# Kernel tuning notes

Measured on AMD Instinct MI355X. Metric: run time of the kernel, lower is better.

## Reference

```python
import jax, jax.numpy as jnp
import numpy as np

N_NODES = 40000
N_EDGES = 640000
D_FEAT = 128


def setup_inputs() -> dict:
    key = jax.random.key(0)
    k1, k2, k3, k4, k5 = jax.random.split(key, 5)
    x = jax.random.normal(k1, (N_NODES, D_FEAT), dtype=jnp.float32)
    edge_rows = jax.random.randint(k2, (N_EDGES,), 0, N_NODES, dtype=jnp.int32)
    edge_cols = jax.random.randint(k3, (N_EDGES,), 0, N_NODES, dtype=jnp.int32)
    adj_vals = jax.random.uniform(k4, (N_EDGES,), dtype=jnp.float32)
    bias = jax.random.normal(k5, (D_FEAT,), dtype=jnp.float32)
    return {"x": x, "edge_rows": edge_rows, "edge_cols": edge_cols,
            "adj_vals": adj_vals, "bias": bias}


def reference(x, edge_rows, edge_cols, adj_vals, bias):
    # SpMM: out[r] = sum_e adj_vals[e] * x[edge_cols[e]] for edges with row r
    msgs = adj_vals[:, None] * x[edge_cols]                    # [E, D]
    agg = jax.ops.segment_sum(msgs, edge_rows, num_segments=N_NODES)  # [E,D]->[N,D]
    # degree = sparse row-sum of adj values
    deg = jax.ops.segment_sum(adj_vals, edge_rows, num_segments=N_NODES)  # [N]
    deg = deg[:, None]
    # mean aggregation; rows with zero degree give NaN in torch, masked to 0
    out = jnp.where(deg == 0, 0.0, agg / jnp.where(deg == 0, 1.0, deg))
    return out + bias
```

## Files before the change

### kernel.cpp

```cpp
#include <hip/hip_runtime.h>

#define N_NODES 40000
#define N_EDGES 640000
#define D_FEAT  128
#define CAP     32
#define OCAP    8192
#define NSLICE  8
#define SLICE_NODES 5000
#define NSUB    16
#define NBIN    (NSLICE * NSUB)
#define BIN2    28
#define STAGE_BLOCKS 625
#define HEAVY_BLOCKS NBIN
#define RANGE_MAX 313
#define CONV_BLOCKS_1K 1250
#define SCAN_BLOCK 256
#define N_SCAN_BLOCKS ((N_NODES + SCAN_BLOCK - 1) / SCAN_BLOCK)

typedef float    f32x4 __attribute__((ext_vector_type(4)));

__device__ __forceinline__ unsigned bf16r(float f) {
    unsigned u = __float_as_uint(f);
    return (u + 0x7FFFu + ((u >> 16) & 1u)) >> 16;
}


__global__ __launch_bounds__(256) void stage_kernel(
    const int*   __restrict__ rows,
    const int*   __restrict__ cols,
    const float* __restrict__ vals,
    int*          __restrict__ ocount,
    int2*         __restrict__ overflow,
    uint2*        __restrict__ queue)
{
    __shared__ int   cnt[NBIN];
    __shared__ uint2 bin[NBIN][BIN2];

    for (int i = threadIdx.x; i < NBIN; i += 256) cnt[i] = 0;
    __syncthreads();

    int vidx = blockIdx.x * 256 + threadIdx.x;
    int4   r4 = ((const int4*)  rows)[vidx];
    int4   c4 = ((const int4*)  cols)[vidx];
    float4 v4 = ((const float4*)vals)[vidx];
    int    rr[4] = { r4.x, r4.y, r4.z, r4.w };
    int    cc[4] = { c4.x, c4.y, c4.z, c4.w };
    float  vv[4] = { v4.x, v4.y, v4.z, v4.w };

    #pragma unroll
    for (int j = 0; j < 4; ++j) {
        int r = rr[j];
        unsigned p = ((unsigned)cc[j] << 16) | bf16r(vv[j]);
        int sl  = r / SLICE_NODES;
        int lr  = r - sl * SLICE_NODES;
        int sub = (lr * NSUB) / SLICE_NODES;
        int bi  = sl * NSUB + sub;
        int idx = atomicAdd(&cnt[bi], 1);
        if (idx < BIN2) {
            bin[bi][idx] = make_uint2(p, (unsigned)r);
        } else {
            int o = atomicAdd(ocount, 1);
            if (o < OCAP) overflow[o] = make_int2(r, (int)p);
        }
    }
    __syncthreads();

    int b = blockIdx.x;
    for (int idx = threadIdx.x; idx < NBIN * BIN2; idx += 256) {
        unsigned bi   = (unsigned)idx / BIN2;
        unsigned slot = (unsigned)idx - bi * BIN2;
        int c = min(cnt[bi], BIN2);
        uint2 rec = (slot < (unsigned)c) ? bin[bi][slot]
                                         : make_uint2(0u, 0xFFFFFFFFu);
        queue[((size_t)bi * STAGE_BLOCKS + b) * BIN2 + slot] = rec;
    }
}

__global__ __launch_bounds__(1024) void consume_kernel(
    const float* __restrict__ x,
    const uint2* __restrict__ queue,
    int*          __restrict__ cursors,
    unsigned*     __restrict__ bucket,
    int*          __restrict__ ocount,
    int2*         __restrict__ overflow,
    uint2*        __restrict__ xbf)
{
    int b = blockIdx.x;
    if (b < HEAVY_BLOCKS) {
        int s = b & 7;
        int j = b >> 3;
        int loc0  = (j * SLICE_NODES + NSUB - 1) / NSUB;
        int loc1  = ((j + 1) * SLICE_NODES + NSUB - 1) / NSUB;
        int range = loc1 - loc0;
        int node0 = s * SLICE_NODES + loc0;

        __shared__ int      lcnt[RANGE_MAX];
        __shared__ unsigned lbuck[RANGE_MAX][CAP];

        for (int i = threadIdx.x; i < range; i += 1024) lcnt[i] = 0;
        __syncthreads();

        const uint2* q = queue + (size_t)(s * NSUB + j) * STAGE_BLOCKS * BIN2;
        const int n = STAGE_BLOCKS * BIN2;
        for (int i = threadIdx.x; i < n; i += 1024) {
            uint2 rec = q[i];
            unsigned ln = rec.y - (unsigned)node0;
            if (ln < (unsigned)range) {
                int idx = atomicAdd(&lcnt[ln], 1);
                if (idx < CAP) lbuck[ln][idx] = rec.x;
                else { int o = atomicAdd(ocount, 1);
                       if (o < OCAP) overflow[o] = make_int2((int)rec.y, (int)rec.x); }
            }
        }
        __syncthreads();

        for (int i = threadIdx.x; i < range; i += 1024)
            cursors[node0 + i] = lcnt[i];
        const unsigned* lb = &lbuck[0][0];
        unsigned* gb = bucket + (size_t)node0 * CAP;
        for (int w = threadIdx.x; w < range * CAP; w += 1024)
            gb[w] = lb[w];
        return;
    }
    int idx = (b - HEAVY_BLOCKS) * 1024 + threadIdx.x;
    float4 f = ((const float4*)x)[idx];
    uint2 o;
    o.x = bf16r(f.x) | (bf16r(f.y) << 16);
    o.y = bf16r(f.z) | (bf16r(f.w) << 16);
    xbf[idx] = o;
}

__global__ __launch_bounds__(256, 8) void gather_bf_kernel(
    const uint2*    __restrict__ xbf,
    const int*      __restrict__ cursors,
    const unsigned* __restrict__ bucket,
    const int2*     __restrict__ overflow,
    const float*    __restrict__ bias,
    float*          __restrict__ out)
{
    int b    = blockIdx.x;
    int hw   = threadIdx.x >> 5;
    int lane = threadIdx.x & 31;
    int node = (b & 7) * SLICE_NODES + (b >> 3) * 8 + hw;

    int k = min(cursors[node], CAP);
    const unsigned* base = bucket + (unsigned)node * CAP;

    unsigned ent = (lane < k) ? base[lane] : 0xFFFFFFFFu;

    #pragma unroll
    for (int kk = 2; kk <= 32; kk <<= 1) {
        #pragma unroll
        for (int j = kk >> 1; j > 0; j >>= 1) {
            unsigned other = __shfl_xor(ent, j, 64);
            bool up      = ((lane & kk) == 0);
            bool lower   = ((lane & j) == 0);
            unsigned mn  = min(ent, other), mx = max(ent, other);
            ent = (up == lower) ? mn : mx;
        }
    }

    int wb = threadIdx.x & 32;

    float4 acc0 = make_float4(0.f, 0.f, 0.f, 0.f);
    float4 acc1 = make_float4(0.f, 0.f, 0.f, 0.f);
    float  deg  = 0.f;

    #define ACC(P_, W_, A_)  {                                             \
        float _v = __uint_as_float((P_) << 16);                            \
        float _f0 = __uint_as_float((W_).x << 16);                         \
        float _f1 = __uint_as_float((W_).x & 0xFFFF0000u);                 \
        float _f2 = __uint_as_float((W_).y << 16);                         \
        float _f3 = __uint_as_float((W_).y & 0xFFFF0000u);                 \
        deg += _v;                                                         \
        A_.x += _v * _f0; A_.y += _v * _f1;                                \
        A_.z += _v * _f2; A_.w += _v * _f3; }

    #define PROC(E_, A_)  {                                                \
        unsigned _en = (E_);                                               \
        uint2 _wv = xbf[(_en >> 16) * 32u + (unsigned)lane];               \
        ACC(_en, _wv, A_); }

    int e = 0;
    for (; e + 8 <= k; e += 8) {
        unsigned p0 = __shfl(ent, wb + e,     64);
        unsigned p1 = __shfl(ent, wb + e + 1, 64);
        unsigned p2 = __shfl(ent, wb + e + 2, 64);
        unsigned p3 = __shfl(ent, wb + e + 3, 64);
        unsigned p4 = __shfl(ent, wb + e + 4, 64);
        unsigned p5 = __shfl(ent, wb + e + 5, 64);
        unsigned p6 = __shfl(ent, wb + e + 6, 64);
        unsigned p7 = __shfl(ent, wb + e + 7, 64);
        uint2 w0 = xbf[(p0 >> 16) * 32u + (unsigned)lane];
        uint2 w1 = xbf[(p1 >> 16) * 32u + (unsigned)lane];
        uint2 w2 = xbf[(p2 >> 16) * 32u + (unsigned)lane];
        uint2 w3 = xbf[(p3 >> 16) * 32u + (unsigned)lane];
        uint2 w4 = xbf[(p4 >> 16) * 32u + (unsigned)lane];
        uint2 w5 = xbf[(p5 >> 16) * 32u + (unsigned)lane];
        uint2 w6 = xbf[(p6 >> 16) * 32u + (unsigned)lane];
        uint2 w7 = xbf[(p7 >> 16) * 32u + (unsigned)lane];
        ACC(p0, w0, acc0); ACC(p1, w1, acc1);
        ACC(p2, w2, acc0); ACC(p3, w3, acc1);
        ACC(p4, w4, acc0); ACC(p5, w5, acc1);
        ACC(p6, w6, acc0); ACC(p7, w7, acc1);
    }
    for (; e + 4 <= k; e += 4) {
        unsigned p0 = __shfl(ent, wb + e,     64);
        unsigned p1 = __shfl(ent, wb + e + 1, 64);
        unsigned p2 = __shfl(ent, wb + e + 2, 64);
        unsigned p3 = __shfl(ent, wb + e + 3, 64);
        uint2 w0 = xbf[(p0 >> 16) * 32u + (unsigned)lane];
        uint2 w1 = xbf[(p1 >> 16) * 32u + (unsigned)lane];
        uint2 w2 = xbf[(p2 >> 16) * 32u + (unsigned)lane];
        uint2 w3 = xbf[(p3 >> 16) * 32u + (unsigned)lane];
        ACC(p0, w0, acc0); ACC(p1, w1, acc1);
        ACC(p2, w2, acc0); ACC(p3, w3, acc1);
    }
    for (; e < k; ++e) {
        unsigned p = __shfl(ent, wb + e, 64);
        PROC(p, acc0);
    }

    int oc = min(cursors[N_NODES], OCAP);
    for (int i = 0; i < oc; ++i) {
        int2 entv = overflow[i];
        if (entv.x == node) PROC((unsigned)entv.y, acc0);
    }
    #undef PROC
    #undef ACC

    float inv = (deg == 0.f) ? 0.f : 1.f / deg;
    float4 bv = ((const float4*)bias)[lane];
    f32x4 ov;
    ov.x = (acc0.x + acc1.x) * inv + bv.x;
    ov.y = (acc0.y + acc1.y) * inv + bv.y;
    ov.z = (acc0.z + acc1.z) * inv + bv.z;
    ov.w = (acc0.w + acc1.w) * inv + bv.w;
    __builtin_nontemporal_store(ov, (f32x4*)(out + (size_t)node * D_FEAT) + lane);
}


__global__ __launch_bounds__(256) void histogram_kernel(
    const int* __restrict__ rows, int* __restrict__ counts)
{
    int e = blockIdx.x * blockDim.x + threadIdx.x;
    if (e < N_EDGES) atomicAdd(&counts[rows[e]], 1);
}

__global__ __launch_bounds__(SCAN_BLOCK) void scan1_kernel(
    const int* __restrict__ counts, int* __restrict__ offsets, int* __restrict__ blocksums)
{
    __shared__ int tmp[SCAN_BLOCK];
    int t = threadIdx.x;
    int g = blockIdx.x * SCAN_BLOCK + t;
    int v = (g < N_NODES) ? counts[g] : 0;
    tmp[t] = v;
    __syncthreads();
    #pragma unroll
    for (int off = 1; off < SCAN_BLOCK; off <<= 1) {
        int add = (t >= off) ? tmp[t - off] : 0;
        __syncthreads();
        tmp[t] += add;
        __syncthreads();
    }
    if (g < N_NODES) offsets[g] = tmp[t] - v;
    if (t == SCAN_BLOCK - 1) blocksums[blockIdx.x] = tmp[t];
}

__global__ __launch_bounds__(SCAN_BLOCK) void scan2_kernel(int* __restrict__ blocksums)
{
    __shared__ int tmp[SCAN_BLOCK];
    int t = threadIdx.x;
    int v = (t < N_SCAN_BLOCKS) ? blocksums[t] : 0;
    tmp[t] = v;
    __syncthreads();
    #pragma unroll
    for (int off = 1; off < SCAN_BLOCK; off <<= 1) {
        int add = (t >= off) ? tmp[t - off] : 0;
        __syncthreads();
        tmp[t] += add;
        __syncthreads();
    }
    if (t < N_SCAN_BLOCKS) blocksums[t] = tmp[t] - v;
}

__global__ __launch_bounds__(SCAN_BLOCK) void scan3_kernel(
    int* __restrict__ offsets, int* __restrict__ cursors, const int* __restrict__ blocksums)
{
    int t = threadIdx.x;
    int g = blockIdx.x * SCAN_BLOCK + t;
    if (g < N_NODES) {
        int o = offsets[g] + blocksums[blockIdx.x];
        offsets[g] = o;
        cursors[g] = o;
    }
    if (g == 0) offsets[N_NODES] = N_EDGES;
}

__global__ __launch_bounds__(256) void bucket_kernel(
    const int* __restrict__ rows, const int* __restrict__ cols,
    const float* __restrict__ vals, int* __restrict__ cursors, int2* __restrict__ bucket)
{
    int e = blockIdx.x * blockDim.x + threadIdx.x;
    if (e >= N_EDGES) return;
    int r = rows[e];
    int pos = atomicAdd(&cursors[r], 1);
    bucket[pos] = make_int2(cols[e], __float_as_int(vals[e]));
}

__global__ __launch_bounds__(256) void gather_csr_kernel(
    const float* __restrict__ x, const int* __restrict__ offsets,
    const int2* __restrict__ bucket, const float* __restrict__ bias,
    float* __restrict__ out)
{
    int t = blockIdx.x * blockDim.x + threadIdx.x;
    int node = t >> 5;
    if (node >= N_NODES) return;
    int lane = t & 31;
    int beg = offsets[node];
    int end = offsets[node + 1];
    float4 acc = make_float4(0.f, 0.f, 0.f, 0.f);
    float deg = 0.f;
    int2 ent = (beg < end) ? bucket[beg] : make_int2(0, 0);
    for (int e = beg; e < end; ++e) {
        int2 cur = ent;
        if (e + 1 < end) ent = bucket[e + 1];
        float v = __int_as_float(cur.y);
        deg += v;
        float4 xv = ((const float4*)(x + (size_t)cur.x * D_FEAT))[lane];
        acc.x += v * xv.x; acc.y += v * xv.y; acc.z += v * xv.z; acc.w += v * xv.w;
    }
    float inv = (deg == 0.f) ? 0.f : 1.f / deg;
    float4 bv = ((const float4*)bias)[lane];
    float4 ov;
    ov.x = acc.x * inv + bv.x; ov.y = acc.y * inv + bv.y;
    ov.z = acc.z * inv + bv.z; ov.w = acc.w * inv + bv.w;
    ((float4*)(out + (size_t)node * D_FEAT))[lane] = ov;
}


__global__ __launch_bounds__(256) void edge_scatter_kernel(
    const float* __restrict__ x, const int* __restrict__ rows,
    const int* __restrict__ cols, const float* __restrict__ vals,
    float* __restrict__ agg, float* __restrict__ deg)
{
    int t = blockIdx.x * blockDim.x + threadIdx.x;
    int edge = t >> 5;
    if (edge >= N_EDGES) return;
    int lane = t & 31;
    int row = rows[edge]; int col = cols[edge]; float v = vals[edge];
    float4 xv = ((const float4*)(x + (size_t)col * D_FEAT))[lane];
    float* dst = agg + (size_t)row * D_FEAT + lane * 4;
    unsafeAtomicAdd(dst + 0, v * xv.x);
    unsafeAtomicAdd(dst + 1, v * xv.y);
    unsafeAtomicAdd(dst + 2, v * xv.z);
    unsafeAtomicAdd(dst + 3, v * xv.w);
    if (lane == 0) unsafeAtomicAdd(deg + row, v);
}

__global__ __launch_bounds__(256) void finalize_kernel(
    float* __restrict__ out, const float* __restrict__ deg, const float* __restrict__ bias)
{
    int t = blockIdx.x * blockDim.x + threadIdx.x;
    int node = t >> 5;
    if (node >= N_NODES) return;
    int lane = t & 31;
    float d = deg[node];
    float inv = (d == 0.f) ? 0.f : 1.f / d;
    float4* o = (float4*)(out + (size_t)node * D_FEAT) + lane;
    float4 bv = ((const float4*)bias)[lane];
    float4 ov = *o;
    ov.x = ov.x * inv + bv.x; ov.y = ov.y * inv + bv.y;
    ov.z = ov.z * inv + bv.z; ov.w = ov.w * inv + bv.w;
    *o = ov;
}


extern "C" void kernel_launch(void* const* d_in, const int* in_sizes, int n_in,
                              void* d_out, int out_size, void* d_ws, size_t ws_size,
                              hipStream_t stream) {
    const float* x    = (const float*)d_in[0];
    const int*   rows = (const int*)  d_in[1];
    const int*   cols = (const int*)  d_in[2];
    const float* vals = (const float*)d_in[3];
    const float* bias = (const float*)d_in[4];
    float* out = (float*)d_out;

    char* wb = (char*)d_ws;
    int*      f_cursors  = (int*)     wb;
    int*      f_ocount   = (int*)    (wb + (size_t)N_NODES * 4);
    int2*     f_overflow = (int2*)   (wb + 160128);
    uint2*    f_xbf      = (uint2*)  (wb + 225792);
    unsigned* f_bucket   = (unsigned*)(wb + 10465792);
    uint2*    f_queue    = (uint2*)  (wb + 15585792);
    size_t need_fast = 15585792 + (size_t)NBIN * STAGE_BLOCKS * BIN2 * 8;

    int* w = (int*)d_ws;
    size_t need_csr = ((size_t)120448 + 2u * N_EDGES) * sizeof(int);

    if (ws_size >= need_fast) {
        (void)hipMemsetAsync(f_ocount, 0, 4, stream);
        stage_kernel<<<STAGE_BLOCKS, 256, 0, stream>>>(
            rows, cols, vals, f_ocount, f_overflow, f_queue);
        consume_kernel<<<HEAVY_BLOCKS + CONV_BLOCKS_1K, 1024, 0, stream>>>(
            x, f_queue, f_cursors, f_bucket, f_ocount, f_overflow, f_xbf);
        gather_bf_kernel<<<N_NODES / 8, 256, 0, stream>>>(
            f_xbf, f_cursors, f_bucket, f_overflow, bias, out);
    } else if (ws_size >= need_csr) {
        int*  counts    = w;
        int*  offsets   = w + 40064;
        int*  cursors   = w + 80128;
        int*  blocksums = w + 120128;
        int2* bucket    = (int2*)(w + 120448);
        (void)hipMemsetAsync(counts, 0, N_NODES * sizeof(int), stream);
        histogram_kernel<<<(N_EDGES + 255) / 256, 256, 0, stream>>>(rows, counts);
        scan1_kernel<<<N_SCAN_BLOCKS, SCAN_BLOCK, 0, stream>>>(counts, offsets, blocksums);
        scan2_kernel<<<1, SCAN_BLOCK, 0, stream>>>(blocksums);
        scan3_kernel<<<N_SCAN_BLOCKS, SCAN_BLOCK, 0, stream>>>(offsets, cursors, blocksums);
        bucket_kernel<<<(N_EDGES + 255) / 256, 256, 0, stream>>>(rows, cols, vals, cursors, bucket);
        int threads = N_NODES * 32;
        gather_csr_kernel<<<(threads + 255) / 256, 256, 0, stream>>>(x, offsets, bucket, bias, out);
    } else {
        float* deg = (float*)d_ws;
        (void)hipMemsetAsync(out, 0, (size_t)N_NODES * D_FEAT * sizeof(float), stream);
        (void)hipMemsetAsync(deg, 0, (size_t)N_NODES * sizeof(float), stream);
        int et = N_EDGES * 32;
        edge_scatter_kernel<<<(et + 255) / 256, 256, 0, stream>>>(x, rows, cols, vals, out, deg);
        int nt = N_NODES * 32;
        finalize_kernel<<<(nt + 255) / 256, 256, 0, stream>>>(out, deg, bias);
    }
}
```

Before: 120.0 us.

## Compact staging queue with global tail atomics and split bf16 conversion across kernels

The stage kernel now reserves space in per-bin global queues with one atomic per bin per block and writes records directly into a compact queue. Before, each block wrote fixed 28-slot padded sub-bins, so consumers had to scan 625*28 records per bin, mostly padding. Part of the x-to-bf16 conversion moves into the stage kernel as extra blocks, leaving only the remainder for the consume kernel, which should balance the two launches. The cost is global atomic contention on 128 tails and a fixed queue capacity per bin, with excess records falling back to the overflow path.

After: 132.2 us. 1.1x slower.

```diff
diff --git a/kernel.cpp b/kernel.cpp
--- a/kernel.cpp
+++ b/kernel.cpp
@@ -9,11 +9,12 @@
 #define SLICE_NODES 5000
 #define NSUB    16
 #define NBIN    (NSLICE * NSUB)
-#define BIN2    28
+#define QCAP    6144
 #define STAGE_BLOCKS 625
+#define STAGE_CONV 2500
 #define HEAVY_BLOCKS NBIN
+#define CONSUME_CONV 625
 #define RANGE_MAX 313
-#define CONV_BLOCKS_1K 1250
 #define SCAN_BLOCK 256
 #define N_SCAN_BLOCKS ((N_NODES + SCAN_BLOCK - 1) / SCAN_BLOCK)
 
@@ -29,17 +30,31 @@
     const int*   __restrict__ rows,
     const int*   __restrict__ cols,
     const float* __restrict__ vals,
+    const float* __restrict__ x,
     int*          __restrict__ ocount,
     int2*         __restrict__ overflow,
-    uint2*        __restrict__ queue)
-{
-    __shared__ int   cnt[NBIN];
-    __shared__ uint2 bin[NBIN][BIN2];
+    int*          __restrict__ tails,
+    uint2*        __restrict__ queue,
+    uint2*        __restrict__ xbf)
+{
+    int b = blockIdx.x;
+    if (b >= STAGE_BLOCKS) {
+        int idx = (b - STAGE_BLOCKS) * 256 + threadIdx.x;
+        float4 f = ((const float4*)x)[idx];
+        uint2 o;
+        o.x = bf16r(f.x) | (bf16r(f.y) << 16);
+        o.y = bf16r(f.z) | (bf16r(f.w) << 16);
+        xbf[idx] = o;
+        return;
+    }
+
+    __shared__ int cnt[NBIN];
+    __shared__ int gbase[NBIN];
 
     for (int i = threadIdx.x; i < NBIN; i += 256) cnt[i] = 0;
     __syncthreads();
 
-    int vidx = blockIdx.x * 256 + threadIdx.x;
+    int vidx = b * 256 + threadIdx.x;
     int4   r4 = ((const int4*)  rows)[vidx];
     int4   c4 = ((const int4*)  cols)[vidx];
     float4 v4 = ((const float4*)vals)[vidx];
@@ -47,37 +62,40 @@
     int    cc[4] = { c4.x, c4.y, c4.z, c4.w };
     float  vv[4] = { v4.x, v4.y, v4.z, v4.w };
 
+    int      bi[4];
+    int      li[4];
+    unsigned pk[4];
     #pragma unroll
     for (int j = 0; j < 4; ++j) {
         int r = rr[j];
-        unsigned p = ((unsigned)cc[j] << 16) | bf16r(vv[j]);
+        pk[j] = ((unsigned)cc[j] << 16) | bf16r(vv[j]);
         int sl  = r / SLICE_NODES;
         int lr  = r - sl * SLICE_NODES;
         int sub = (lr * NSUB) / SLICE_NODES;
-        int bi  = sl * NSUB + sub;
-        int idx = atomicAdd(&cnt[bi], 1);
-        if (idx < BIN2) {
-            bin[bi][idx] = make_uint2(p, (unsigned)r);
+        bi[j] = sl * NSUB + sub;
+        li[j] = atomicAdd(&cnt[bi[j]], 1);
+    }
+    __syncthreads();
+
+    if (threadIdx.x < NBIN)
+        gbase[threadIdx.x] = atomicAdd(&tails[threadIdx.x], cnt[threadIdx.x]);
+    __syncthreads();
+
+    #pragma unroll
+    for (int j = 0; j < 4; ++j) {
+        int gpos = gbase[bi[j]] + li[j];
+        if (gpos < QCAP) {
+            queue[(size_t)bi[j] * QCAP + gpos] = make_uint2(pk[j], (unsigned)rr[j]);
         } else {
             int o = atomicAdd(ocount, 1);
-            if (o < OCAP) overflow[o] = make_int2(r, (int)p);
+            if (o < OCAP) overflow[o] = make_int2(rr[j], (int)pk[j]);
         }
-    }
-    __syncthreads();
-
-    int b = blockIdx.x;
-    for (int idx = threadIdx.x; idx < NBIN * BIN2; idx += 256) {
-        unsigned bi   = (unsigned)idx / BIN2;
-        unsigned slot = (unsigned)idx - bi * BIN2;
-        int c = min(cnt[bi], BIN2);
-        uint2 rec = (slot < (unsigned)c) ? bin[bi][slot]
-                                         : make_uint2(0u, 0xFFFFFFFFu);
-        queue[((size_t)bi * STAGE_BLOCKS + b) * BIN2 + slot] = rec;
     }
 }
 
 __global__ __launch_bounds__(1024) void consume_kernel(
     const float* __restrict__ x,
+    const int*   __restrict__ tails,
     const uint2* __restrict__ queue,
     int*          __restrict__ cursors,
     unsigned*     __restrict__ bucket,
@@ -100,8 +118,9 @@
         for (int i = threadIdx.x; i < range; i += 1024) lcnt[i] = 0;
         __syncthreads();
 
-        const uint2* q = queue + (size_t)(s * NSUB + j) * STAGE_BLOCKS * BIN2;
-        const int n = STAGE_BLOCKS * BIN2;
+        int bin = s * NSUB + j;
+        int n = min(tails[bin], QCAP);
+        const uint2* q = queue + (size_t)bin * QCAP;
         for (int i = threadIdx.x; i < n; i += 1024) {
             uint2 rec = q[i];
             unsigned ln = rec.y - (unsigned)node0;
@@ -122,7 +141,7 @@
             gb[w] = lb[w];
         return;
     }
-    int idx = (b - HEAVY_BLOCKS) * 1024 + threadIdx.x;
+    int idx = 640000 + (b - HEAVY_BLOCKS) * 1024 + threadIdx.x;
     float4 f = ((const float4*)x)[idx];
     uint2 o;
     o.x = bf16r(f.x) | (bf16r(f.y) << 16);
@@ -389,21 +408,22 @@
     char* wb = (char*)d_ws;
     int*      f_cursors  = (int*)     wb;
     int*      f_ocount   = (int*)    (wb + (size_t)N_NODES * 4);
-    int2*     f_overflow = (int2*)   (wb + 160128);
-    uint2*    f_xbf      = (uint2*)  (wb + 225792);
-    unsigned* f_bucket   = (unsigned*)(wb + 10465792);
-    uint2*    f_queue    = (uint2*)  (wb + 15585792);
-    size_t need_fast = 15585792 + (size_t)NBIN * STAGE_BLOCKS * BIN2 * 8;
+    int*      f_tails    = (int*)    (wb + 160032);
+    int2*     f_overflow = (int2*)   (wb + 160640);
+    uint2*    f_xbf      = (uint2*)  (wb + 226304);
+    unsigned* f_bucket   = (unsigned*)(wb + 10466304);
+    uint2*    f_queue    = (uint2*)  (wb + 15586304);
+    size_t need_fast = 15586304 + (size_t)NBIN * QCAP * 8;
 
     int* w = (int*)d_ws;
     size_t need_csr = ((size_t)120448 + 2u * N_EDGES) * sizeof(int);
 
     if (ws_size >= need_fast) {
-        (void)hipMemsetAsync(f_ocount, 0, 4, stream);
-        stage_kernel<<<STAGE_BLOCKS, 256, 0, stream>>>(
-            rows, cols, vals, f_ocount, f_overflow, f_queue);
-        consume_kernel<<<HEAVY_BLOCKS + CONV_BLOCKS_1K, 1024, 0, stream>>>(
-            x, f_queue, f_cursors, f_bucket, f_ocount, f_overflow, f_xbf);
+        (void)hipMemsetAsync(wb + 160000, 0, 544, stream);
+        stage_kernel<<<STAGE_BLOCKS + STAGE_CONV, 256, 0, stream>>>(
+            rows, cols, vals, x, f_ocount, f_overflow, f_tails, f_queue, f_xbf);
+        consume_kernel<<<HEAVY_BLOCKS + CONSUME_CONV, 1024, 0, stream>>>(
+            x, f_tails, f_queue, f_cursors, f_bucket, f_ocount, f_overflow, f_xbf);
         gather_bf_kernel<<<N_NODES / 8, 256, 0, stream>>>(
             f_xbf, f_cursors, f_bucket, f_overflow, bias, out);
     } else if (ws_size >= need_csr) {
```
